# Kernel tuning notes

Measured on AMD Instinct MI355X. Metric: run time of the kernel, lower is better.

Reference implementation:

```python
import jax, jax.numpy as jnp
import numpy as np

K = 3  # kernel_size
KK = K * K


def conv2d(x, w, b, stride=1, padding=1, dilation=1):
    out = jax.lax.conv_general_dilated(
        x, w, (stride, stride), [(padding, padding), (padding, padding)],
        rhs_dilation=(dilation, dilation),
        dimension_numbers=('NCHW', 'OIHW', 'NCHW'))
    return out + b[None, :, None, None]


def bilinear_gather(x, py, px):
    # x: [B,C,H,W]; py,px: [B,KK,H,W] float sampling coords (zero outside).
    B, C, H, W = x.shape
    y0 = jnp.floor(py)
    x0 = jnp.floor(px)
    wy1 = py - y0
    wx1 = px - x0
    xf = x.reshape(B, C, H * W)

    def corner(yc, xc, wgt):
        valid = (yc >= 0) & (yc <= H - 1) & (xc >= 0) & (xc <= W - 1)
        yi = jnp.clip(yc, 0, H - 1).astype(jnp.int32)
        xi = jnp.clip(xc, 0, W - 1).astype(jnp.int32)
        idx = (yi * W + xi).reshape(B, 1, -1)  # [B,1,KK*H*W]
        v = jnp.take_along_axis(xf, jnp.broadcast_to(idx, (B, C, idx.shape[-1])), axis=2)
        v = v.reshape(B, C, *yc.shape[1:])  # [B,C,KK,H,W]
        return v * (wgt * valid)[:, None]

    return (corner(y0, x0, (1 - wy1) * (1 - wx1)) +
            corner(y0, x0 + 1, (1 - wy1) * wx1) +
            corner(y0 + 1, x0, wy1 * (1 - wx1)) +
            corner(y0 + 1, x0 + 1, wy1 * wx1))


def modulated_deform_conv(x, offset, mask, w, b, stride=1, padding=1, dilation=1):
    B, C, H, W = x.shape
    Ho, Wo = offset.shape[2], offset.shape[3]
    off = offset.reshape(B, KK, 2, Ho, Wo)
    dy, dx = off[:, :, 0], off[:, :, 1]  # [B,KK,Ho,Wo]
    ki, kj = jnp.meshgrid(jnp.arange(K), jnp.arange(K), indexing='ij')
    ki = ki.reshape(-1).astype(x.dtype)  # [KK]
    kj = kj.reshape(-1).astype(x.dtype)
    base_y = (jnp.arange(Ho) * stride - padding).astype(x.dtype)
    base_x = (jnp.arange(Wo) * stride - padding).astype(x.dtype)
    py = base_y[None, None, :, None] + (ki * dilation)[None, :, None, None] + dy
    px = base_x[None, None, None, :] + (kj * dilation)[None, :, None, None] + dx
    x_off = bilinear_gather(x, py, px)              # [B,C,KK,Ho,Wo]
    x_off = x_off * mask[:, None]                   # modulation
    w_flat = w.reshape(w.shape[0], C, KK)           # [O,C,KK]
    out = jnp.einsum('bckhw,ock->bohw', x_off, w_flat)
    return out + b[None, :, None, None]


def setup_inputs() -> dict:
    key = jax.random.key(0)
    ks = jax.random.split(key, 7)
    B, C, O, H, W = 8, 64, 64, 128, 128
    x = jax.random.normal(ks[0], (B, C, H, W), dtype=jnp.float32)
    # offset/mask predictor convs (zero-init in the module; randomized small here
    # so offsets/masks are non-trivial for kernel correctness testing)
    p_w = jax.random.normal(ks[1], (2 * KK, C, 3, 3), dtype=jnp.float32) * 0.02
    p_b = jax.random.normal(ks[2], (2 * KK,), dtype=jnp.float32) * 0.1
    m_w = jax.random.normal(ks[3], (KK, C, 3, 3), dtype=jnp.float32) * 0.02
    m_b = jax.random.normal(ks[4], (KK,), dtype=jnp.float32) * 0.1
    # deformable conv weights
    d_w = jax.random.normal(ks[5], (O, C, K, K), dtype=jnp.float32) * (1.0 / np.sqrt(C * KK))
    d_b = jax.random.normal(ks[6], (O,), dtype=jnp.float32) * 0.01
    return {"x": x, "p_w": p_w, "p_b": p_b, "m_w": m_w, "m_b": m_b, "d_w": d_w, "d_b": d_b}


def reference(x, p_w, p_b, m_w, m_b, d_w, d_b):
    offset = conv2d(x, p_w, p_b, stride=1, padding=1, dilation=1)   # [B,18,H,W]
    mask = jax.nn.sigmoid(conv2d(x, m_w, m_b, stride=1, padding=1, dilation=1))  # [B,9,H,W]
    out = modulated_deform_conv(x, offset, mask, d_w, d_b, stride=1, padding=1, dilation=1)
    return (out, offset)
```

## Files before the change

### kernel.cpp

```cpp
#include <hip/hip_runtime.h>
#include <math.h>

#define KK 9
#define BB 8
#define CC 64
#define OO 64
#define HH 128
#define WW 128
#define HWSZ (HH*WW)

typedef _Float16 half8 __attribute__((ext_vector_type(8)));
typedef float    floatx4 __attribute__((ext_vector_type(4)));

#define WP_ELEMS (9*2*4*32*8)
#define WD_ELEMS (9*2*4*64*8)
#define XH_ELEMS ((size_t)BB*HWSZ*64)
#define NCONV 2048

__global__ __launch_bounds__(256) void prep(
    const float* __restrict__ x,
    const float* __restrict__ p_w, const float* __restrict__ m_w,
    const float* __restrict__ d_w,
    _Float16* __restrict__ Wp, _Float16* __restrict__ Wd, _Float16* __restrict__ x_h,
    int conv_blocks)
{
    const int blk = blockIdx.x;
    const int tid = threadIdx.x;
    if (blk < conv_blocks) {
        __shared__ _Float16 sh[64][72];
        const int b    = blk >> 8;
        const int pix0 = (blk & 255) * 64;
        const float* xb = x + (size_t)b*CC*HWSZ + pix0;
        {
            const int f  = tid & 15;
            const int c0 = tid >> 4;
            #pragma unroll
            for (int j = 0; j < 4; ++j) {
                const int c = j*16 + c0;
                const floatx4 v = *(const floatx4*)(xb + (size_t)c*HWSZ + f*4);
                sh[f*4+0][c] = (_Float16)v[0];
                sh[f*4+1][c] = (_Float16)v[1];
                sh[f*4+2][c] = (_Float16)v[2];
                sh[f*4+3][c] = (_Float16)v[3];
            }
        }
        __syncthreads();
        {
            const int p  = tid >> 2;
            const int c0 = (tid & 3) * 16;
            _Float16* dst = x_h + ((size_t)b*HWSZ + pix0 + p)*64 + c0;
            *(half8*)dst       = *(const half8*)&sh[p][c0];
            *(half8*)(dst + 8) = *(const half8*)&sh[p][c0 + 8];
        }
    } else {
        const int i = (blk - conv_blocks)*256 + tid;
        if (i < WP_ELEMS) {
            const int e = i & 7, n = (i>>3)&31, quad = (i>>8)&3, ks = (i>>10)&1, k = i>>11;
            const int c = ks*32 + quad*8 + e;
            float v = 0.f;
            if (n < 18)      v = p_w[(n*CC + c)*KK + k];
            else if (n < 27) v = m_w[((n-18)*CC + c)*KK + k];
            Wp[i] = (_Float16)v;
        } else if (i < WP_ELEMS + WD_ELEMS) {
            const int j = i - WP_ELEMS;
            const int e = j & 7, o = (j>>3)&63, quad = (j>>9)&3, ks = (j>>11)&1, k = j>>12;
            const int c = ks*32 + quad*8 + e;
            Wd[j] = (_Float16)d_w[(o*CC + c)*KK + k];
        }
    }
}

__global__ __launch_bounds__(256, 3) void dcn_fused(
    const _Float16* __restrict__ x_h,
    const _Float16* __restrict__ Wp, const _Float16* __restrict__ Wd,
    const float* __restrict__ p_b, const float* __restrict__ m_b,
    const float* __restrict__ db,
    float* __restrict__ out, float* __restrict__ offset_out)
{
    __shared__ alignas(16) float T[27*68];

    const int tid  = threadIdx.x;
    const int wv   = tid >> 6;
    const int lane = tid & 63;
    const int quad = lane >> 4;
    const int l15  = lane & 15;
    const int b    = blockIdx.x & 7;
    const int seg  = blockIdx.x >> 3;
    const int row  = seg >> 1;
    const int col0 = (seg & 1) * 64;
    const int pix0 = row * WW + col0;
    const _Float16* xbh = x_h + (size_t)b*HWSZ*64;

    const int p2   = wv*16 + (lane >> 2);
    const int part = lane & 3;
    const int wx2  = col0 + p2;
    const int bidx = ((l15 << 2) | quad) << 2;

    union U { half8 h; int i[4]; };

    floatx4 accp[2];
    accp[0] = (floatx4)0.f; accp[1] = (floatx4)0.f;
    #pragma unroll
    for (int k = 0; k < 9; ++k) {
        const int hy = row + k/3 - 1;
        const int hx = wx2 + k%3 - 1;
        const bool vld = (hy >= 0) & (hy < HH) & (hx >= 0) & (hx < WW);
        const _Float16* ap = xbh + (size_t)(vld ? hy*WW + hx : 0)*64 + part*8;
        const half8 z = (half8)(_Float16)0.f;
        half8 a0 = *(const half8*)ap;
        half8 a1 = *(const half8*)(ap + 32);
        a0 = vld ? a0 : z;
        a1 = vld ? a1 : z;
        U u0, u1, b0, b1;
        u0.h = a0; u1.h = a1;
        #pragma unroll
        for (int d = 0; d < 4; ++d) {
            b0.i[d] = __builtin_amdgcn_ds_bpermute(bidx, u0.i[d]);
            b1.i[d] = __builtin_amdgcn_ds_bpermute(bidx, u1.i[d]);
        }
        const _Float16* wp = Wp + k*2048 + quad*256 + l15*8;
        accp[0] = __builtin_amdgcn_mfma_f32_16x16x32_f16(b0.h, *(const half8*)(wp),              accp[0], 0, 0, 0);
        accp[1] = __builtin_amdgcn_mfma_f32_16x16x32_f16(b0.h, *(const half8*)(wp + 128),        accp[1], 0, 0, 0);
        accp[0] = __builtin_amdgcn_mfma_f32_16x16x32_f16(b1.h, *(const half8*)(wp + 1024),       accp[0], 0, 0, 0);
        accp[1] = __builtin_amdgcn_mfma_f32_16x16x32_f16(b1.h, *(const half8*)(wp + 1024 + 128), accp[1], 0, 0, 0);
    }

    #pragma unroll
    for (int nt = 0; nt < 2; ++nt) {
        const int ch = nt*16 + l15;
        if (ch < 27) {
            const float bias = (ch < 18) ? p_b[ch] : m_b[ch-18];
            #pragma unroll
            for (int r = 0; r < 4; ++r)
                T[ch*68 + wv*16 + quad*4 + r] = accp[nt][r] + bias;
        }
    }
    __syncthreads();

    {
        float* offp = offset_out + (size_t)b*18*HWSZ + pix0;
        #pragma unroll
        for (int j = 0; j < 5; ++j) {
            const int idx = j*256 + tid;
            if (idx < 18*64) {
                const int ch = idx >> 6, pp = idx & 63;
                offp[ch*HWSZ + pp] = T[ch*68 + pp];
            }
        }
    }
    float dyk[9], dxk[9], mkk[9];
    #pragma unroll
    for (int k = 0; k < 9; ++k) {
        dyk[k] = T[(2*k  )*68 + p2];
        dxk[k] = T[(2*k+1)*68 + p2];
        mkk[k] = 1.f / (1.f + expf(-T[(18+k)*68 + p2]));
    }

    floatx4 acc[4];
    #pragma unroll
    for (int nt = 0; nt < 4; ++nt) acc[nt] = (floatx4)0.f;

    half8 GA[8], GB[8];
    _Float16 gA[4], gB[4];

    #define ISSUE(kk, G, g) do {                                                   \
        const float py  = (float)(row - 1 + (kk)/3) + dyk[kk];                     \
        const float pxf = (float)(wx2 - 1 + (kk)%3) + dxk[kk];                     \
        const float y0f = floorf(py), x0f = floorf(pxf);                           \
        const int   iy0 = (int)y0f,   ix0 = (int)x0f;                              \
        const float wy1 = py - y0f,   wx1 = pxf - x0f;                             \
        const float wy0 = 1.f - wy1,  wx0 = 1.f - wx1;                             \
        const bool vy0 = ((unsigned)iy0     < (unsigned)HH);                       \
        const bool vy1 = ((unsigned)(iy0+1) < (unsigned)HH);                       \
        const bool vx0 = ((unsigned)ix0     < (unsigned)WW);                       \
        const bool vx1 = ((unsigned)(ix0+1) < (unsigned)WW);                       \
        const int cy0 = min(max(iy0,   0), HH-1), cy1 = min(max(iy0+1, 0), HH-1);  \
        const int cx0 = min(max(ix0,   0), WW-1), cx1 = min(max(ix0+1, 0), WW-1);  \
        const float mk = mkk[kk];                                                  \
        g[0] = (_Float16)(wy0*wx0*((vy0&vx0) ? mk : 0.f));                         \
        g[1] = (_Float16)(wy0*wx1*((vy0&vx1) ? mk : 0.f));                         \
        g[2] = (_Float16)(wy1*wx0*((vy1&vx0) ? mk : 0.f));                         \
        g[3] = (_Float16)(wy1*wx1*((vy1&vx1) ? mk : 0.f));                         \
        const _Float16* c0p = xbh + (size_t)(cy0*WW+cx0)*64 + part*8;              \
        const _Float16* c1p = xbh + (size_t)(cy0*WW+cx1)*64 + part*8;              \
        const _Float16* c2p = xbh + (size_t)(cy1*WW+cx0)*64 + part*8;              \
        const _Float16* c3p = xbh + (size_t)(cy1*WW+cx1)*64 + part*8;              \
        G[0] = *(const half8*)c0p;  G[1] = *(const half8*)(c0p + 32);              \
        G[2] = *(const half8*)c1p;  G[3] = *(const half8*)(c1p + 32);              \
        G[4] = *(const half8*)c2p;  G[5] = *(const half8*)(c2p + 32);              \
        G[6] = *(const half8*)c3p;  G[7] = *(const half8*)(c3p + 32);              \
    } while (0)

    #define CONSUME(kk, G, g) do {                                                 \
        const half8 lo = G[0]*g[0] + G[2]*g[1] + G[4]*g[2] + G[6]*g[3];            \
        const half8 hi = G[1]*g[0] + G[3]*g[1] + G[5]*g[2] + G[7]*g[3];            \
        U ulo, uhi, a0u, a1u;                                                      \
        ulo.h = lo; uhi.h = hi;                                                    \
        _Pragma("unroll")                                                          \
        for (int d = 0; d < 4; ++d) {                                              \
            a0u.i[d] = __builtin_amdgcn_ds_bpermute(bidx, ulo.i[d]);               \
            a1u.i[d] = __builtin_amdgcn_ds_bpermute(bidx, uhi.i[d]);               \
        }                                                                          \
        const _Float16* wd0 = Wd + (kk)*4096 +        quad*512 + l15*8;            \
        const _Float16* wd1 = Wd + (kk)*4096 + 2048 + quad*512 + l15*8;            \
        _Pragma("unroll")                                                          \
        for (int nt = 0; nt < 4; ++nt)                                             \
            acc[nt] = __builtin_amdgcn_mfma_f32_16x16x32_f16(a0u.h, *(const half8*)(wd0 + nt*128), acc[nt], 0, 0, 0); \
        _Pragma("unroll")                                                          \
        for (int nt = 0; nt < 4; ++nt)                                             \
            acc[nt] = __builtin_amdgcn_mfma_f32_16x16x32_f16(a1u.h, *(const half8*)(wd1 + nt*128), acc[nt], 0, 0, 0); \
    } while (0)

    ISSUE(0, GA, gA);
    ISSUE(1, GB, gB);
    CONSUME(0, GA, gA);  ISSUE(2, GA, gA);
    CONSUME(1, GB, gB);  ISSUE(3, GB, gB);
    CONSUME(2, GA, gA);  ISSUE(4, GA, gA);
    CONSUME(3, GB, gB);  ISSUE(5, GB, gB);
    CONSUME(4, GA, gA);  ISSUE(6, GA, gA);
    CONSUME(5, GB, gB);  ISSUE(7, GB, gB);
    CONSUME(6, GA, gA);  ISSUE(8, GA, gA);
    CONSUME(7, GB, gB);
    CONSUME(8, GA, gA);

    #undef ISSUE
    #undef CONSUME

    __syncthreads();
    float* T2 = T;
    #pragma unroll
    for (int oc = 0; oc < 4; ++oc) {
        #pragma unroll
        for (int r = 0; r < 4; ++r)
            T2[l15*68 + wv*16 + quad*4 + r] = acc[oc][r];
        __syncthreads();
        #pragma unroll
        for (int j = 0; j < 4; ++j) {
            const int idx = j*256 + tid;
            const int o16 = idx >> 6, pp = idx & 63;
            out[((size_t)b*OO + oc*16 + o16)*HWSZ + pix0 + pp] = T2[o16*68 + pp] + db[oc*16 + o16];
        }
        __syncthreads();
    }
}

__global__ __launch_bounds__(256, 4) void dcn_fused_lds(
    const float* __restrict__ x,
    const _Float16* __restrict__ Wp, const _Float16* __restrict__ Wd,
    const float* __restrict__ p_b, const float* __restrict__ m_b,
    const float* __restrict__ db,
    float* __restrict__ out, float* __restrict__ offset_out)
{
    __shared__ alignas(16) _Float16 A_sh[128][72];
    __shared__ alignas(16) _Float16 WM_sh[32*72];
    __shared__ alignas(16) _Float16 Wd_sh[64][72];

    const int tid   = threadIdx.x;
    const int wv    = tid >> 6;
    const int lane  = tid & 63;
    const int quad  = lane >> 4;
    const int l15   = lane & 15;
    const int b     = blockIdx.x & 7;
    const int row   = blockIdx.x >> 3;
    const int pix0  = row * WW;
    const int p     = tid & 127;
    const int chalf = (tid >> 7) * 32;
    const int h = row, w = p;
    const float* xb = x + (size_t)b*CC*HWSZ;
    _Float16 (*W_sh)[72] = (_Float16 (*)[72])WM_sh;

    floatx4 accp[2][2];
    #pragma unroll
    for (int mt = 0; mt < 2; ++mt)
        #pragma unroll
        for (int nt = 0; nt < 2; ++nt) accp[mt][nt] = (floatx4)0.f;

    for (int k = 0; k < 9; ++k) {
        {
            const int n  = tid >> 3;
            const int c0 = (tid & 7) * 8;
            *(half8*)&W_sh[n][c0] =
                *(const half8*)(Wp + k*2048 + (c0>>5)*1024 + ((c0>>3)&3)*256 + n*8);
        }
        const int hy = h + (k/3) - 1;
        const int wx = w + (k%3) - 1;
        const bool vld = (hy >= 0) & (hy < HH) & (wx >= 0) & (wx < WW);
        const float* xs = xb + hy*WW + wx;
        #pragma unroll
        for (int cb = 0; cb < 4; ++cb) {
            union { half8 v; _Float16 e[8]; } u;
            #pragma unroll
            for (int j = 0; j < 8; ++j)
                u.e[j] = (_Float16)(vld ? xs[(size_t)(chalf + cb*8 + j)*HWSZ] : 0.f);
            *(half8*)&A_sh[p][chalf + cb*8] = u.v;
        }
        __syncthreads();
        #pragma unroll
        for (int ks = 0; ks < 2; ++ks) {
            half8 bf[2];
            #pragma unroll
            for (int nt = 0; nt < 2; ++nt)
                bf[nt] = *(const half8*)&W_sh[nt*16 + l15][ks*32 + quad*8];
            #pragma unroll
            for (int mt = 0; mt < 2; ++mt) {
                half8 af = *(const half8*)&A_sh[wv*32 + mt*16 + l15][ks*32 + quad*8];
                accp[mt][0] = __builtin_amdgcn_mfma_f32_16x16x32_f16(af, bf[0], accp[mt][0], 0, 0, 0);
                accp[mt][1] = __builtin_amdgcn_mfma_f32_16x16x32_f16(af, bf[1], accp[mt][1], 0, 0, 0);
            }
        }
        __syncthreads();
    }

    float (*T)[132] = (float (*)[132])&A_sh[0][0];
    #pragma unroll
    for (int nt = 0; nt < 2; ++nt) {
        const int ch = nt*16 + l15;
        if (ch < 27) {
            #pragma unroll
            for (int mt = 0; mt < 2; ++mt)
                #pragma unroll
                for (int r = 0; r < 4; ++r)
                    T[ch][wv*32 + mt*16 + quad*4 + r] = accp[mt][nt][r];
        }
    }
    __syncthreads();

    float dyk[9], dxk[9], mkk[9];
    float* offp = offset_out + (size_t)b*18*HWSZ + pix0;
    #pragma unroll
    for (int k = 0; k < 9; ++k) {
        dyk[k] = T[2*k][p]   + p_b[2*k];
        dxk[k] = T[2*k+1][p] + p_b[2*k+1];
        mkk[k] = 1.f / (1.f + expf(-(T[18+k][p] + m_b[k])));
    }
    if (tid < 128) {
        #pragma unroll
        for (int k = 0; k < 9; ++k) {
            offp[(2*k  )*HWSZ + p] = dyk[k];
            offp[(2*k+1)*HWSZ + p] = dxk[k];
        }
    }
    __syncthreads();

    floatx4 acc[2][4];
    #pragma unroll
    for (int mt = 0; mt < 2; ++mt)
        #pragma unroll
        for (int nt = 0; nt < 4; ++nt) acc[mt][nt] = (floatx4)0.f;

    for (int k = 0; k < 9; ++k) {
        {
            const int o  = tid >> 2;
            const int c0 = (tid & 3) * 16;
            *(half8*)&Wd_sh[o][c0] =
                *(const half8*)(Wd + k*4096 + (c0>>5)*2048 + ((c0>>3)&3)*512 + o*8);
            const int c8 = c0 + 8;
            *(half8*)&Wd_sh[o][c8] =
                *(const half8*)(Wd + k*4096 + (c8>>5)*2048 + ((c8>>3)&3)*512 + o*8);
        }
        const float mk = mkk[k];
        const float py = (float)(h - 1 + k/3) + dyk[k];
        const float px = (float)(w - 1 + k%3) + dxk[k];
        const float y0f = floorf(py), x0f = floorf(px);
        const int   iy0 = (int)y0f,   ix0 = (int)x0f;
        const float wy1 = py - y0f,   wx1 = px - x0f;
        const float wy0 = 1.f - wy1,  wx0 = 1.f - wx1;
        const bool vy0 = (iy0   >= 0) & (iy0   < HH);
        const bool vy1 = (iy0+1 >= 0) & (iy0+1 < HH);
        const bool vx0 = (ix0   >= 0) & (ix0   < WW);
        const bool vx1 = (ix0+1 >= 0) & (ix0+1 < WW);
        const int cy0 = min(max(iy0,   0), HH-1), cy1 = min(max(iy0+1, 0), HH-1);
        const int cx0 = min(max(ix0,   0), WW-1), cx1 = min(max(ix0+1, 0), WW-1);
        const int i0 = cy0*WW+cx0; const float w0 = wy0*wx0*((vy0&vx0) ? mk : 0.f);
        const int i1 = cy0*WW+cx1; const float w1 = wy0*wx1*((vy0&vx1) ? mk : 0.f);
        const int i2 = cy1*WW+cx0; const float w2 = wy1*wx0*((vy1&vx0) ? mk : 0.f);
        const int i3 = cy1*WW+cx1; const float w3 = wy1*wx1*((vy1&vx1) ? mk : 0.f);
        #pragma unroll
        for (int cb = 0; cb < 4; ++cb) {
            union { half8 v; _Float16 e[8]; } u;
            #pragma unroll
            for (int j = 0; j < 8; ++j) {
                const float* xc = xb + (size_t)(chalf + cb*8 + j)*HWSZ;
                u.e[j] = (_Float16)(w0*xc[i0] + w1*xc[i1] + w2*xc[i2] + w3*xc[i3]);
            }
            *(half8*)&A_sh[p][chalf + cb*8] = u.v;
        }
        __syncthreads();
        #pragma unroll
        for (int ks = 0; ks < 2; ++ks) {
            half8 bf[4];
            #pragma unroll
            for (int nt = 0; nt < 4; ++nt)
                bf[nt] = *(const half8*)&Wd_sh[nt*16 + l15][ks*32 + quad*8];
            #pragma unroll
            for (int mt = 0; mt < 2; ++mt) {
                half8 af = *(const half8*)&A_sh[wv*32 + mt*16 + l15][ks*32 + quad*8];
                #pragma unroll
                for (int nt = 0; nt < 4; ++nt)
                    acc[mt][nt] = __builtin_amdgcn_mfma_f32_16x16x32_f16(af, bf[nt], acc[mt][nt], 0, 0, 0);
            }
        }
        __syncthreads();
    }

    float (*T2)[132] = (float (*)[132])&A_sh[0][0];
    #pragma unroll
    for (int oc = 0; oc < 4; ++oc) {
        #pragma unroll
        for (int mt = 0; mt < 2; ++mt)
            #pragma unroll
            for (int r = 0; r < 4; ++r)
                T2[l15][wv*32 + mt*16 + quad*4 + r] = acc[mt][oc][r];
        __syncthreads();
        #pragma unroll
        for (int j = 0; j < 8; ++j) {
            const int idx = tid + j*256;
            const int o16 = idx >> 7, pp = idx & 127;
            out[((size_t)b*OO + oc*16 + o16)*HWSZ + pix0 + pp] = T2[o16][pp] + db[oc*16 + o16];
        }
        __syncthreads();
    }
}

extern "C" void kernel_launch(void* const* d_in, const int* in_sizes, int n_in,
                              void* d_out, int out_size, void* d_ws, size_t ws_size,
                              hipStream_t stream) {
    const float* x   = (const float*)d_in[0];
    const float* p_w = (const float*)d_in[1];
    const float* p_b = (const float*)d_in[2];
    const float* m_w = (const float*)d_in[3];
    const float* m_b = (const float*)d_in[4];
    const float* dw  = (const float*)d_in[5];
    const float* db  = (const float*)d_in[6];

    float* out        = (float*)d_out;
    float* offset_out = out + (size_t)BB*OO*HWSZ;

    _Float16* Wp  = (_Float16*)d_ws;
    _Float16* Wd  = Wp + WP_ELEMS;
    _Float16* x_h = Wd + WD_ELEMS;

    const int nrep = (WP_ELEMS + WD_ELEMS + 255) / 256;
    const size_t need = (size_t)(WP_ELEMS + WD_ELEMS + XH_ELEMS) * sizeof(_Float16);
    if (ws_size >= need) {
        prep<<<dim3(NCONV + nrep), 256, 0, stream>>>(x, p_w, m_w, dw, Wp, Wd, x_h, NCONV);
        dcn_fused<<<dim3(256*BB), 256, 0, stream>>>(x_h, Wp, Wd, p_b, m_b, db, out, offset_out);
    } else {
        prep<<<dim3(nrep), 256, 0, stream>>>(x, p_w, m_w, dw, Wp, Wd, x_h, 0);
        dcn_fused_lds<<<dim3(128*BB), 256, 0, stream>>>(x, Wp, Wd, p_b, m_b, db, out, offset_out);
    }
}
```

Baseline: 148.8 us.

## Split deform conv into two channel passes with LDS-staged weights and triple-buffered gathers

Splits the bilinear-gather plus MFMA loop into two passes over channel halves. Each pass stages its half of the deform-conv weights into shared memory instead of reading them from global memory per MFMA. Gathers are issued through inline-asm loads with explicit vmcnt waits across three rotating buffers, which keeps more loads in flight with fewer registers per buffer. In exchange, every corner address is computed twice and more barriers are added, and the shared memory footprint grows to about 36KB, which may limit occupancy.

```diff
diff --git a/kernel.cpp b/kernel.cpp
--- a/kernel.cpp
+++ b/kernel.cpp
@@ -77,7 +77,9 @@
     const float* __restrict__ db,
     float* __restrict__ out, float* __restrict__ offset_out)
 {
-    __shared__ alignas(16) float T[27*68];
+    __shared__ alignas(16) char smem[9*2048*2];
+    _Float16* WL = (_Float16*)smem;
+    float*    T  = (float*)smem;
 
     const int tid  = threadIdx.x;
     const int wv   = tid >> 6;
@@ -155,79 +157,99 @@
         dxk[k] = T[(2*k+1)*68 + p2];
         mkk[k] = 1.f / (1.f + expf(-T[(18+k)*68 + p2]));
     }
+    __syncthreads();
 
     floatx4 acc[4];
     #pragma unroll
     for (int nt = 0; nt < 4; ++nt) acc[nt] = (floatx4)0.f;
 
-    half8 GA[8], GB[8];
-    _Float16 gA[4], gB[4];
-
-    #define ISSUE(kk, G, g) do {                                                   \
-        const float py  = (float)(row - 1 + (kk)/3) + dyk[kk];                     \
-        const float pxf = (float)(wx2 - 1 + (kk)%3) + dxk[kk];                     \
-        const float y0f = floorf(py), x0f = floorf(pxf);                           \
-        const int   iy0 = (int)y0f,   ix0 = (int)x0f;                              \
-        const float wy1 = py - y0f,   wx1 = pxf - x0f;                             \
-        const float wy0 = 1.f - wy1,  wx0 = 1.f - wx1;                             \
-        const bool vy0 = ((unsigned)iy0     < (unsigned)HH);                       \
-        const bool vy1 = ((unsigned)(iy0+1) < (unsigned)HH);                       \
-        const bool vx0 = ((unsigned)ix0     < (unsigned)WW);                       \
-        const bool vx1 = ((unsigned)(ix0+1) < (unsigned)WW);                       \
-        const int cy0 = min(max(iy0,   0), HH-1), cy1 = min(max(iy0+1, 0), HH-1);  \
-        const int cx0 = min(max(ix0,   0), WW-1), cx1 = min(max(ix0+1, 0), WW-1);  \
-        const float mk = mkk[kk];                                                  \
-        g[0] = (_Float16)(wy0*wx0*((vy0&vx0) ? mk : 0.f));                         \
-        g[1] = (_Float16)(wy0*wx1*((vy0&vx1) ? mk : 0.f));                         \
-        g[2] = (_Float16)(wy1*wx0*((vy1&vx0) ? mk : 0.f));                         \
-        g[3] = (_Float16)(wy1*wx1*((vy1&vx1) ? mk : 0.f));                         \
-        const _Float16* c0p = xbh + (size_t)(cy0*WW+cx0)*64 + part*8;              \
-        const _Float16* c1p = xbh + (size_t)(cy0*WW+cx1)*64 + part*8;              \
-        const _Float16* c2p = xbh + (size_t)(cy1*WW+cx0)*64 + part*8;              \
-        const _Float16* c3p = xbh + (size_t)(cy1*WW+cx1)*64 + part*8;              \
-        G[0] = *(const half8*)c0p;  G[1] = *(const half8*)(c0p + 32);              \
-        G[2] = *(const half8*)c1p;  G[3] = *(const half8*)(c1p + 32);              \
-        G[4] = *(const half8*)c2p;  G[5] = *(const half8*)(c2p + 32);              \
-        G[6] = *(const half8*)c3p;  G[7] = *(const half8*)(c3p + 32);              \
+    half8 GA[4], GB[4], GC[4];
+    _Float16 gA[4], gB[4], gC[4];
+
+    #define STAGE(KS) do {                                                          \
+        _Pragma("unroll")                                                           \
+        for (int j = 0; j < 9; ++j) {                                               \
+            const int c   = j*256 + tid;                                            \
+            const int kk  = c >> 8;                                                 \
+            const int rem = c & 255;                                                \
+            *(half8*)&WL[kk*2048 + rem*8] =                                         \
+                *(const half8*)(Wd + kk*4096 + (KS)*2048 + rem*8);                  \
+        }                                                                           \
     } while (0)
 
-    #define CONSUME(kk, G, g) do {                                                 \
-        const half8 lo = G[0]*g[0] + G[2]*g[1] + G[4]*g[2] + G[6]*g[3];            \
-        const half8 hi = G[1]*g[0] + G[3]*g[1] + G[5]*g[2] + G[7]*g[3];            \
-        U ulo, uhi, a0u, a1u;                                                      \
-        ulo.h = lo; uhi.h = hi;                                                    \
-        _Pragma("unroll")                                                          \
-        for (int d = 0; d < 4; ++d) {                                              \
-            a0u.i[d] = __builtin_amdgcn_ds_bpermute(bidx, ulo.i[d]);               \
-            a1u.i[d] = __builtin_amdgcn_ds_bpermute(bidx, uhi.i[d]);               \
-        }                                                                          \
-        const _Float16* wd0 = Wd + (kk)*4096 +        quad*512 + l15*8;            \
-        const _Float16* wd1 = Wd + (kk)*4096 + 2048 + quad*512 + l15*8;            \
-        _Pragma("unroll")                                                          \
-        for (int nt = 0; nt < 4; ++nt)                                             \
-            acc[nt] = __builtin_amdgcn_mfma_f32_16x16x32_f16(a0u.h, *(const half8*)(wd0 + nt*128), acc[nt], 0, 0, 0); \
-        _Pragma("unroll")                                                          \
-        for (int nt = 0; nt < 4; ++nt)                                             \
-            acc[nt] = __builtin_amdgcn_mfma_f32_16x16x32_f16(a1u.h, *(const half8*)(wd1 + nt*128), acc[nt], 0, 0, 0); \
+    #define GISSUE(kk, G, g, KS) do {                                               \
+        const float py  = (float)(row - 1 + (kk)/3) + dyk[kk];                      \
+        const float pxf = (float)(wx2 - 1 + (kk)%3) + dxk[kk];                      \
+        const float y0f = floorf(py), x0f = floorf(pxf);                            \
+        const int   iy0 = (int)y0f,   ix0 = (int)x0f;                               \
+        const float wy1 = py - y0f,   wx1 = pxf - x0f;                              \
+        const float wy0 = 1.f - wy1,  wx0 = 1.f - wx1;                              \
+        const bool vy0 = ((unsigned)iy0     < (unsigned)HH);                        \
+        const bool vy1 = ((unsigned)(iy0+1) < (unsigned)HH);                        \
+        const bool vx0 = ((unsigned)ix0     < (unsigned)WW);                        \
+        const bool vx1 = ((unsigned)(ix0+1) < (unsigned)WW);                        \
+        const int cy0 = min(max(iy0,   0), HH-1), cy1 = min(max(iy0+1, 0), HH-1);   \
+        const int cx0 = min(max(ix0,   0), WW-1), cx1 = min(max(ix0+1, 0), WW-1);   \
+        const float mk = mkk[kk];                                                   \
+        g[0] = (_Float16)(wy0*wx0*((vy0&vx0) ? mk : 0.f));                          \
+        g[1] = (_Float16)(wy0*wx1*((vy0&vx1) ? mk : 0.f));                          \
+        g[2] = (_Float16)(wy1*wx0*((vy1&vx0) ? mk : 0.f));                          \
+        g[3] = (_Float16)(wy1*wx1*((vy1&vx1) ? mk : 0.f));                          \
+        const _Float16* c0p = xbh + (size_t)(cy0*WW+cx0)*64 + (KS)*32 + part*8;     \
+        const _Float16* c1p = xbh + (size_t)(cy0*WW+cx1)*64 + (KS)*32 + part*8;     \
+        const _Float16* c2p = xbh + (size_t)(cy1*WW+cx0)*64 + (KS)*32 + part*8;     \
+        const _Float16* c3p = xbh + (size_t)(cy1*WW+cx1)*64 + (KS)*32 + part*8;     \
+        asm volatile("global_load_dwordx4 %0, %1, off" : "=v"(G[0]) : "v"(c0p));    \
+        asm volatile("global_load_dwordx4 %0, %1, off" : "=v"(G[1]) : "v"(c1p));    \
+        asm volatile("global_load_dwordx4 %0, %1, off" : "=v"(G[2]) : "v"(c2p));    \
+        asm volatile("global_load_dwordx4 %0, %1, off" : "=v"(G[3]) : "v"(c3p));    \
     } while (0)
 
-    ISSUE(0, GA, gA);
-    ISSUE(1, GB, gB);
-    CONSUME(0, GA, gA);  ISSUE(2, GA, gA);
-    CONSUME(1, GB, gB);  ISSUE(3, GB, gB);
-    CONSUME(2, GA, gA);  ISSUE(4, GA, gA);
-    CONSUME(3, GB, gB);  ISSUE(5, GB, gB);
-    CONSUME(4, GA, gA);  ISSUE(6, GA, gA);
-    CONSUME(5, GB, gB);  ISSUE(7, GB, gB);
-    CONSUME(6, GA, gA);  ISSUE(8, GA, gA);
-    CONSUME(7, GB, gB);
-    CONSUME(8, GA, gA);
-
-    #undef ISSUE
-    #undef CONSUME
-
-    __syncthreads();
-    float* T2 = T;
+    #define GW8(G) asm volatile("s_waitcnt vmcnt(8)"  : "+v"(G[0]),"+v"(G[1]),"+v"(G[2]),"+v"(G[3]))
+    #define GW4(G) asm volatile("s_waitcnt vmcnt(4)"  : "+v"(G[0]),"+v"(G[1]),"+v"(G[2]),"+v"(G[3]))
+    #define GW0(G) asm volatile("s_waitcnt vmcnt(0)"  : "+v"(G[0]),"+v"(G[1]),"+v"(G[2]),"+v"(G[3]) :: "memory")
+
+    #define GCONS(kk, G, g) do {                                                    \
+        const half8 lo = G[0]*g[0] + G[1]*g[1] + G[2]*g[2] + G[3]*g[3];             \
+        U ulo, au;  ulo.h = lo;                                                     \
+        _Pragma("unroll")                                                           \
+        for (int d = 0; d < 4; ++d)                                                 \
+            au.i[d] = __builtin_amdgcn_ds_bpermute(bidx, ulo.i[d]);                 \
+        const _Float16* wdp = &WL[(kk)*2048 + quad*512 + l15*8];                    \
+        _Pragma("unroll")                                                           \
+        for (int nt = 0; nt < 4; ++nt)                                              \
+            acc[nt] = __builtin_amdgcn_mfma_f32_16x16x32_f16(au.h, *(const half8*)(wdp + nt*128), acc[nt], 0, 0, 0); \
+    } while (0)
+
+    #define PASS(KS) do {                                                           \
+        STAGE(KS);                                                                  \
+        __syncthreads();                                                            \
+        GISSUE(0, GA, gA, KS);  GISSUE(1, GB, gB, KS);  GISSUE(2, GC, gC, KS);      \
+        GW8(GA); GCONS(0, GA, gA);  GISSUE(3, GA, gA, KS);                          \
+        GW8(GB); GCONS(1, GB, gB);  GISSUE(4, GB, gB, KS);                          \
+        GW8(GC); GCONS(2, GC, gC);  GISSUE(5, GC, gC, KS);                          \
+        GW8(GA); GCONS(3, GA, gA);  GISSUE(6, GA, gA, KS);                          \
+        GW8(GB); GCONS(4, GB, gB);  GISSUE(7, GB, gB, KS);                          \
+        GW8(GC); GCONS(5, GC, gC);  GISSUE(8, GC, gC, KS);                          \
+        GW8(GA); GCONS(6, GA, gA);                                                  \
+        GW4(GB); GCONS(7, GB, gB);                                                  \
+        GW0(GC); GCONS(8, GC, gC);                                                  \
+    } while (0)
+
+    PASS(0);
+    __syncthreads();
+    PASS(1);
+
+    #undef STAGE
+    #undef GISSUE
+    #undef GW8
+    #undef GW4
+    #undef GW0
+    #undef GCONS
+    #undef PASS
+
+    __syncthreads();
+    float* T2 = (float*)smem;
     #pragma unroll
     for (int oc = 0; oc < 4; ++oc) {
         #pragma unroll
```

Result: slower. 168.0 us (+12.9%).
